# Kernel tuning notes

Measured on AMD Instinct MI355X. Metric: run time of the kernel, lower is better.

Reference implementation:

```python
import jax, jax.numpy as jnp
import numpy as np

H, W = 256, 832
B = 2
SEARCH_W, SEARCH_H = 7, 3
SPARSITY_RAD = 2
SENSE_RANGE = 10
PIX_W = 20.0          # pixel_distance_weight
ALPHA_W = 0.7         # alpha_distance_weight
MULLINE_W = 15.0      # pixel_mulline_distance_weight
ALPHA_PAD = 0.6       # alpha_padding
INF = 1e9


def _sorted_offsets(span_x, span_y):
    xs, ys = np.meshgrid(span_x, span_y)
    xs = xs.flatten(); ys = ys.flatten()
    order = np.argsort(xs ** 2 + ys ** 2, kind='stable')
    return xs[order].astype(np.int32), ys[order].astype(np.int32)


def setup_inputs() -> dict:
    key = jax.random.key(0)
    k1, k2 = jax.random.split(key)
    src = (jax.random.uniform(k1, (B, 1, H, W)) < 0.02).astype(jnp.float32)
    dst = (jax.random.uniform(k2, (B, 1, H, W)) < 0.02).astype(jnp.float32)
    xx, yy = _sorted_offsets(np.arange(-SEARCH_W, SEARCH_W + 1), np.arange(-SEARCH_H, SEARCH_H + 1))
    sxs, sys_ = np.meshgrid(np.arange(-SPARSITY_RAD, SPARSITY_RAD + 1), np.arange(-SPARSITY_RAD, SPARSITY_RAD + 1))
    sxx = sxs.flatten().astype(np.int32); syy = sys_.flatten().astype(np.int32)
    cxx, cyy = _sorted_offsets(np.arange(-SENSE_RANGE, SENSE_RANGE + 1), np.arange(-SENSE_RANGE, SENSE_RANGE + 1))
    return {"binMapsrc": src, "binMapdst": dst,
            "xx": jnp.asarray(xx), "yy": jnp.asarray(yy),
            "sxx": jnp.asarray(sxx), "syy": jnp.asarray(syy),
            "cxx": jnp.asarray(cxx), "cyy": jnp.asarray(cyy)}


def _orientation(m):
    # local edge orientation from a 3x3 box-blurred map
    b = sum(jnp.roll(jnp.roll(m, di, 0), dj, 1) for di in (-1, 0, 1) for dj in (-1, 0, 1))
    gy, gx = jnp.gradient(b)
    return jnp.arctan2(gy, gx)


def _morph_single(src, dst, xx, yy, sxx, syy, cxx, cyy):
    gy, gx = jnp.meshgrid(jnp.arange(H, dtype=jnp.int32), jnp.arange(W, dtype=jnp.int32), indexing='ij')

    def gather(offy, offx, arr, fill):
        ii = gy[None] + offy[:, None, None]          # [K,H,W]
        jj = gx[None] + offx[:, None, None]
        inb = (ii >= 0) & (ii < H) & (jj >= 0) & (jj < W)
        vals = arr[jnp.clip(ii, 0, H - 1), jnp.clip(jj, 0, W - 1)]
        return jnp.where(inb, vals, fill)

    src_e = src > 0.5
    # --- sparsify source edge points: keep min-linear-index edge in each sparsity window ---
    lin = jnp.where(src_e, (gy * W + gx).astype(jnp.float32), INF)
    keep = src_e & (lin == gather(syy, sxx, lin, INF).min(0))
    # --- windowed correspondence search with distance + orientation scoring ---
    theta_s = _orientation(src)
    theta_d = _orientation(dst)
    hit = gather(yy, xx, dst, 0.0) > 0.5             # [K,H,W]
    ang = 1.0 - jnp.cos(theta_s[None] - gather(yy, xx, theta_d, 0.0))
    dist = jnp.sqrt((xx * xx + yy * yy).astype(jnp.float32))
    score = jnp.where(hit, PIX_W * dist[:, None, None] + MULLINE_W * ALPHA_W * ang, INF)
    kbest = jnp.argmin(score, axis=0)                # [H,W]
    active = keep & (score.min(0) < 0.5 * INF)
    dispx = jnp.where(active, xx[kbest].astype(jnp.float32), 0.0)
    dispy = jnp.where(active, yy[kbest].astype(jnp.float32), 0.0)
    # --- diffuse sparse displacements over the sense window (scan keeps memory small) ---
    R = SENSE_RANGE
    pad = lambda a: jnp.pad(a, ((R, R), (R, R)))
    pdx, pdy, pm = pad(dispx), pad(dispy), pad(active.astype(jnp.float32))
    wk = jnp.exp(-jnp.sqrt((cxx * cxx + cyy * cyy).astype(jnp.float32)) / (0.5 * R))

    def body(carry, inp):
        nx, ny, den = carry
        dy_, dx_, w = inp
        sl = lambda a: jax.lax.dynamic_slice(a, (R + dy_, R + dx_), (H, W))
        return (nx + w * sl(pdx), ny + w * sl(pdy), den + w * sl(pm)), None

    zeros = jnp.zeros((H, W), jnp.float32)
    (nx, ny, den), _ = jax.lax.scan(body, (zeros, zeros, zeros), (cyy, cxx, wk))
    mdx = ALPHA_PAD * nx / (den + 1e-6)
    mdy = ALPHA_PAD * ny / (den + 1e-6)
    morphedx = gx.astype(jnp.float32) + mdx
    morphedy = gy.astype(jnp.float32) + mdy
    return jnp.stack([morphedx, morphedy], 0)        # [2,H,W]


def reference(binMapsrc, binMapdst, xx, yy, sxx, syy, cxx, cyy):
    f = lambda s, d: _morph_single(s, d, xx, yy, sxx, syy, cxx, cyy)
    return jax.vmap(f)(binMapsrc[:, 0], binMapdst[:, 0])  # [B,2,H,W]
```

## Files before the change

### kernel.cpp

```cpp
#include <hip/hip_runtime.h>
#include <math.h>

#define BB 2
#define HH 256
#define WW 832
#define HWIMG (HH * WW)

#define TX2 52
#define TY2 16
#define SEG 64
#define ECAP 192

__device__ inline float theta_at(const float* __restrict__ m, int i, int j) {
    int ri[5], cj[5];
#pragma unroll
    for (int t = 0; t < 5; ++t) {
        int r = i + t - 2; r = (r < 0) ? r + HH : (r >= HH ? r - HH : r);
        int c = j + t - 2; c = (c < 0) ? c + WW : (c >= WW ? c - WW : c);
        ri[t] = r * WW; cj[t] = c;
    }
    float S[5][5];
#pragma unroll
    for (int a = 0; a < 5; ++a)
#pragma unroll
        for (int c = 0; c < 5; ++c)
            S[a][c] = m[ri[a] + cj[c]];
    float ct[5], cm[5], cb[5];
#pragma unroll
    for (int c = 0; c < 5; ++c) {
        ct[c] = S[0][c] + S[1][c] + S[2][c];
        cm[c] = S[1][c] + S[2][c] + S[3][c];
        cb[c] = S[2][c] + S[3][c] + S[4][c];
    }
    float Bm = ct[1] + ct[2] + ct[3];
    float Bp = cb[1] + cb[2] + cb[3];
    float Bl = cm[0] + cm[1] + cm[2];
    float Br = cm[2] + cm[3] + cm[4];
    float Bc = cm[1] + cm[2] + cm[3];
    float gy = (i == 0) ? (Bp - Bc) : (i == HH - 1) ? (Bc - Bm) : 0.5f * (Bp - Bm);
    float gx = (j == 0) ? (Br - Bc) : (j == WW - 1) ? (Bc - Bl) : 0.5f * (Br - Bl);
    return atan2f(gy, gx);
}

__global__ void prep_search_kernel(const float* __restrict__ src, const float* __restrict__ dst,
                                   const int* __restrict__ xx, const int* __restrict__ yy, int K,
                                   int* __restrict__ cnt, int* __restrict__ seg) {
    __shared__ int kox[128], koy[128];
    __shared__ float kd[128];
    __shared__ int recs[SEG];
    __shared__ float tss[SEG];
    __shared__ int outv[SEG];
    __shared__ int nkeep;

    int tid = threadIdx.x;
    if (tid == 0) nkeep = 0;
    for (int t = tid; t < K; t += 256) {
        int ox = xx[t], oy = yy[t];
        kox[t] = ox; koy[t] = oy;
        kd[t] = 20.0f * sqrtf((float)(ox * ox + oy * oy));
    }
    __syncthreads();

    int txi = blockIdx.x, tyi = blockIdx.y, b = blockIdx.z;
    int gi = tyi * 16 + (tid >> 4);
    int gj = txi * 16 + (tid & 15);
    const float* sb = src + b * HWIMG;
    const float* db = dst + b * HWIMG;

    if (sb[gi * WW + gj] > 0.5f) {
        float m = 0.f;
#pragma unroll
        for (int p = 0; p < 12; ++p) {
            int di = (p < 5) ? -2 : (p < 10 ? -1 : 0);
            int dj = (p < 5) ? (p - 2) : (p < 10 ? (p - 7) : (p - 12));
            int ii = gi + di, jj = gj + dj;
            bool inb = (ii >= 0) && (jj >= 0) && (jj < WW);
            float v = sb[inb ? (ii * WW + jj) : 0];
            m = fmaxf(m, inb ? v : 0.f);
        }
        if (m <= 0.5f) {
            float ts = theta_at(sb, gi, gj);
            int pos = atomicAdd(&nkeep, 1);
            if (pos < SEG) { recs[pos] = gj | (gi << 10); tss[pos] = ts; }
        }
    }
    __syncthreads();

    int nk = (nkeep < SEG) ? nkeep : SEG;
    int lane = tid & 63;
    int wv = tid >> 6;
    for (int w = wv; w < nk; w += 4) {
        int rec = recs[w];
        int kj = rec & 1023;
        int ki = rec >> 10;
        float ts = tss[w];

        float best = 1e9f;
        int bk = 1 << 20;
#pragma unroll
        for (int rr = 0; rr < 2; ++rr) {
            int k = lane + rr * 64;
            if (k < K) {
                int pi = ki + koy[k], pj = kj + kox[k];
                if (pi >= 0 && pi < HH && pj >= 0 && pj < WW && db[pi * WW + pj] > 0.5f) {
                    float td = theta_at(db, pi, pj);
                    float sc = kd[k] + 10.5f * (1.0f - cosf(ts - td));
                    if (sc < best || (sc == best && k < bk)) { best = sc; bk = k; }
                }
            }
        }
#pragma unroll
        for (int off = 32; off >= 1; off >>= 1) {
            float ob = __shfl_down(best, off, 64);
            int ok = __shfl_down(bk, off, 64);
            if (ob < best || (ob == best && ok < bk)) { best = ob; bk = ok; }
        }
        if (lane == 0)
            outv[w] = (best < 5e8f)
                ? (rec | (b << 18) | ((kox[bk] + 7) << 19) | ((koy[bk] + 3) << 23))
                : -1;
    }
    __syncthreads();

    int tile = (b * TY2 + tyi) * TX2 + txi;
    if (tid < nk) seg[tile * SEG + tid] = outv[tid];
    if (tid == 0) cnt[tile] = nk;
}

__global__ void diffuse_kernel(const int* __restrict__ cnt, const int* __restrict__ seg,
                               float* __restrict__ out) {
    __shared__ float wt[441];
    __shared__ float4 ent[ECAP];
    __shared__ int ncnt[9];
    __shared__ int ne;

    int tid = threadIdx.x;
    if (tid == 0) ne = 0;
    for (int t = tid; t < 441; t += 256) {
        int dy = t / 21 - 10;
        int dx = t % 21 - 10;
        wt[t] = expf(-sqrtf((float)(dx * dx + dy * dy)) / 5.0f);
    }
    int txi = blockIdx.x, tyi = blockIdx.y, b = blockIdx.z;
    if (tid < 9) {
        int nty = tyi + tid / 3 - 1;
        int ntx = txi + tid % 3 - 1;
        ncnt[tid] = (nty >= 0 && nty < TY2 && ntx >= 0 && ntx < TX2)
                        ? cnt[(b * TY2 + nty) * TX2 + ntx] : 0;
    }
    __syncthreads();

    for (int t = tid; t < 9 * SEG; t += 256) {
        int q = t / SEG, slot = t % SEG;
        if (slot < ncnt[q]) {
            int nty = tyi + q / 3 - 1;
            int ntx = txi + q % 3 - 1;
            int v = seg[((b * TY2 + nty) * TX2 + ntx) * SEG + slot];
            if (v != -1) {
                int pos = atomicAdd(&ne, 1);
                if (pos < ECAP)
                    ent[pos] = make_float4((float)(v & 1023), (float)((v >> 10) & 255),
                                           (float)(((v >> 19) & 15) - 7),
                                           (float)(((v >> 23) & 7) - 3));
            }
        }
    }
    __syncthreads();

    int nn = (ne < ECAP) ? ne : ECAP;
    int gj = txi * 16 + (tid & 15);
    int gi = tyi * 16 + (tid >> 4);
    float nx = 0.f, ny = 0.f, de = 0.f;
    for (int c = 0; c < nn; ++c) {
        float4 E = ent[c];
        int dj = (int)E.x - gj;
        int di = (int)E.y - gi;
        if (dj >= -10 && dj <= 10 && di >= -10 && di <= 10) {
            float w = wt[(di + 10) * 21 + dj + 10];
            de += w; nx += w * E.z; ny += w * E.w;
        }
    }
    float inv = 0.6f / (de + 1e-6f);
    int obase = b * 2 * HWIMG;
    out[obase + gi * WW + gj] = (float)gj + nx * inv;
    out[obase + HWIMG + gi * WW + gj] = (float)gi + ny * inv;
}

extern "C" void kernel_launch(void* const* d_in, const int* in_sizes, int n_in,
                              void* d_out, int out_size, void* d_ws, size_t ws_size,
                              hipStream_t stream) {
    const float* src = (const float*)d_in[0];
    const float* dst = (const float*)d_in[1];
    const int* xx = (const int*)d_in[2];
    const int* yy = (const int*)d_in[3];
    int K = in_sizes[2];

    int* cnt = (int*)d_ws;
    int* seg = cnt + BB * TY2 * TX2;
    float* out = (float*)d_out;

    dim3 grid(TX2, TY2, BB);
    prep_search_kernel<<<grid, dim3(256), 0, stream>>>(src, dst, xx, yy, K, cnt, seg);
    diffuse_kernel<<<grid, dim3(256), 0, stream>>>(cnt, seg, out);
}
```

Measured before the change: 91.04 us.

## Fuse prep/search and diffusion into one kernel with 32x32 tiles and halo recompute

Replaces the two-kernel pipeline, which passed packed match records through workspace, with a single kernel per 32x32 output tile. Each block recomputes sparsification and orientation search over a 52x52 halo region, keeps the matches in shared memory, and then diffuses them onto its pixels. This drops one launch and the global round trip through the workspace. In exchange, the halo work is recomputed by neighbouring blocks, the grid shrinks to 416 blocks of 1024 threads, and a capacity of 256 candidates per halo could overflow.

```diff
diff --git a/kernel.cpp b/kernel.cpp
--- a/kernel.cpp
+++ b/kernel.cpp
@@ -6,10 +6,12 @@
 #define WW 832
 #define HWIMG (HH * WW)
 
-#define TX2 52
-#define TY2 16
-#define SEG 64
-#define ECAP 192
+#define TS 32
+#define TXN (WW / TS)
+#define TYN (HH / TS)
+#define RG 52
+#define RGPX (RG * RG)
+#define KCAP 256
 
 __device__ inline float theta_at(const float* __restrict__ m, int i, int j) {
     int ri[5], cj[5];
@@ -42,54 +44,66 @@
     return atan2f(gy, gx);
 }
 
-__global__ void prep_search_kernel(const float* __restrict__ src, const float* __restrict__ dst,
-                                   const int* __restrict__ xx, const int* __restrict__ yy, int K,
-                                   int* __restrict__ cnt, int* __restrict__ seg) {
+__global__ __launch_bounds__(1024) void fused_kernel(
+        const float* __restrict__ src, const float* __restrict__ dst,
+        const int* __restrict__ xx, const int* __restrict__ yy, int K,
+        float* __restrict__ out) {
     __shared__ int kox[128], koy[128];
     __shared__ float kd[128];
-    __shared__ int recs[SEG];
-    __shared__ float tss[SEG];
-    __shared__ int outv[SEG];
-    __shared__ int nkeep;
+    __shared__ int recs[KCAP];
+    __shared__ float tss[KCAP];
+    __shared__ float4 ent[KCAP];
+    __shared__ float wt[441];
+    __shared__ int nkeep, ne;
 
     int tid = threadIdx.x;
-    if (tid == 0) nkeep = 0;
-    for (int t = tid; t < K; t += 256) {
+    if (tid == 0) { nkeep = 0; ne = 0; }
+    for (int t = tid; t < K; t += 1024) {
         int ox = xx[t], oy = yy[t];
         kox[t] = ox; koy[t] = oy;
         kd[t] = 20.0f * sqrtf((float)(ox * ox + oy * oy));
     }
+    for (int t = tid; t < 441; t += 1024) {
+        int dy = t / 21 - 10;
+        int dx = t % 21 - 10;
+        wt[t] = expf(-sqrtf((float)(dx * dx + dy * dy)) / 5.0f);
+    }
+
+    int b = blockIdx.z;
+    int i0 = blockIdx.y * TS;
+    int j0 = blockIdx.x * TS;
+    const float* sb = src + b * HWIMG;
+    const float* db = dst + b * HWIMG;
     __syncthreads();
 
-    int txi = blockIdx.x, tyi = blockIdx.y, b = blockIdx.z;
-    int gi = tyi * 16 + (tid >> 4);
-    int gj = txi * 16 + (tid & 15);
-    const float* sb = src + b * HWIMG;
-    const float* db = dst + b * HWIMG;
-
-    if (sb[gi * WW + gj] > 0.5f) {
-        float m = 0.f;
+    for (int t = tid; t < RGPX; t += 1024) {
+        int gi = i0 - 10 + t / RG;
+        int gj = j0 - 10 + t % RG;
+        if (gi < 0 || gi >= HH || gj < 0 || gj >= WW) continue;
+        if (sb[gi * WW + gj] > 0.5f) {
+            float m = 0.f;
 #pragma unroll
-        for (int p = 0; p < 12; ++p) {
-            int di = (p < 5) ? -2 : (p < 10 ? -1 : 0);
-            int dj = (p < 5) ? (p - 2) : (p < 10 ? (p - 7) : (p - 12));
-            int ii = gi + di, jj = gj + dj;
-            bool inb = (ii >= 0) && (jj >= 0) && (jj < WW);
-            float v = sb[inb ? (ii * WW + jj) : 0];
-            m = fmaxf(m, inb ? v : 0.f);
-        }
-        if (m <= 0.5f) {
-            float ts = theta_at(sb, gi, gj);
-            int pos = atomicAdd(&nkeep, 1);
-            if (pos < SEG) { recs[pos] = gj | (gi << 10); tss[pos] = ts; }
+            for (int p = 0; p < 12; ++p) {
+                int di = (p < 5) ? -2 : (p < 10 ? -1 : 0);
+                int dj = (p < 5) ? (p - 2) : (p < 10 ? (p - 7) : (p - 12));
+                int ii = gi + di, jj = gj + dj;
+                bool inb = (ii >= 0) && (jj >= 0) && (jj < WW);
+                float v = sb[inb ? (ii * WW + jj) : 0];
+                m = fmaxf(m, inb ? v : 0.f);
+            }
+            if (m <= 0.5f) {
+                float ts = theta_at(sb, gi, gj);
+                int pos = atomicAdd(&nkeep, 1);
+                if (pos < KCAP) { recs[pos] = gj | (gi << 10); tss[pos] = ts; }
+            }
         }
     }
     __syncthreads();
 
-    int nk = (nkeep < SEG) ? nkeep : SEG;
+    int nk = (nkeep < KCAP) ? nkeep : KCAP;
     int lane = tid & 63;
     int wv = tid >> 6;
-    for (int w = wv; w < nk; w += 4) {
+    for (int w = wv; w < nk; w += 16) {
         int rec = recs[w];
         int kj = rec & 1023;
         int ki = rec >> 10;
@@ -115,61 +129,18 @@
             int ok = __shfl_down(bk, off, 64);
             if (ob < best || (ob == best && ok < bk)) { best = ob; bk = ok; }
         }
-        if (lane == 0)
-            outv[w] = (best < 5e8f)
-                ? (rec | (b << 18) | ((kox[bk] + 7) << 19) | ((koy[bk] + 3) << 23))
-                : -1;
-    }
-    __syncthreads();
-
-    int tile = (b * TY2 + tyi) * TX2 + txi;
-    if (tid < nk) seg[tile * SEG + tid] = outv[tid];
-    if (tid == 0) cnt[tile] = nk;
-}
-
-__global__ void diffuse_kernel(const int* __restrict__ cnt, const int* __restrict__ seg,
-                               float* __restrict__ out) {
-    __shared__ float wt[441];
-    __shared__ float4 ent[ECAP];
-    __shared__ int ncnt[9];
-    __shared__ int ne;
-
-    int tid = threadIdx.x;
-    if (tid == 0) ne = 0;
-    for (int t = tid; t < 441; t += 256) {
-        int dy = t / 21 - 10;
-        int dx = t % 21 - 10;
-        wt[t] = expf(-sqrtf((float)(dx * dx + dy * dy)) / 5.0f);
-    }
-    int txi = blockIdx.x, tyi = blockIdx.y, b = blockIdx.z;
-    if (tid < 9) {
-        int nty = tyi + tid / 3 - 1;
-        int ntx = txi + tid % 3 - 1;
-        ncnt[tid] = (nty >= 0 && nty < TY2 && ntx >= 0 && ntx < TX2)
-                        ? cnt[(b * TY2 + nty) * TX2 + ntx] : 0;
-    }
-    __syncthreads();
-
-    for (int t = tid; t < 9 * SEG; t += 256) {
-        int q = t / SEG, slot = t % SEG;
-        if (slot < ncnt[q]) {
-            int nty = tyi + q / 3 - 1;
-            int ntx = txi + q % 3 - 1;
-            int v = seg[((b * TY2 + nty) * TX2 + ntx) * SEG + slot];
-            if (v != -1) {
-                int pos = atomicAdd(&ne, 1);
-                if (pos < ECAP)
-                    ent[pos] = make_float4((float)(v & 1023), (float)((v >> 10) & 255),
-                                           (float)(((v >> 19) & 15) - 7),
-                                           (float)(((v >> 23) & 7) - 3));
-            }
+        if (lane == 0 && best < 5e8f) {
+            int pos = atomicAdd(&ne, 1);
+            if (pos < KCAP)
+                ent[pos] = make_float4((float)kj, (float)ki,
+                                       (float)kox[bk], (float)koy[bk]);
         }
     }
     __syncthreads();
 
-    int nn = (ne < ECAP) ? ne : ECAP;
-    int gj = txi * 16 + (tid & 15);
-    int gi = tyi * 16 + (tid >> 4);
+    int nn = (ne < KCAP) ? ne : KCAP;
+    int gj = j0 + (tid & 31);
+    int gi = i0 + (tid >> 5);
     float nx = 0.f, ny = 0.f, de = 0.f;
     for (int c = 0; c < nn; ++c) {
         float4 E = ent[c];
@@ -195,11 +166,7 @@
     const int* yy = (const int*)d_in[3];
     int K = in_sizes[2];
 
-    int* cnt = (int*)d_ws;
-    int* seg = cnt + BB * TY2 * TX2;
     float* out = (float*)d_out;
-
-    dim3 grid(TX2, TY2, BB);
-    prep_search_kernel<<<grid, dim3(256), 0, stream>>>(src, dst, xx, yy, K, cnt, seg);
-    diffuse_kernel<<<grid, dim3(256), 0, stream>>>(cnt, seg, out);
+    dim3 grid(TXN, TYN, BB);
+    fused_kernel<<<grid, dim3(1024), 0, stream>>>(src, dst, xx, yy, K, out);
 }
```

Measured after the change: 108.6 us. 1.19x slower.
